# Kernel optimization log

Hardware: AMD Instinct MI355X
Metric: run time of the kernel (lower is better)

## Reference

```python
import jax, jax.numpy as jnp
import numpy as np

K_NN = 9  # neighbors including self (init kwarg K)
EPS = 1e-12  # F.normalize eps


def setup_inputs() -> dict:
    key = jax.random.key(0)
    ks = jax.random.split(key, 6)
    b, c, t = 8, 64, 4096
    c_out = 64
    x = jax.random.normal(ks[0], (b, c, t), dtype=jnp.float32)
    scale = 1.0 / np.sqrt(c)
    Wq = jax.random.normal(ks[1], (c, c), dtype=jnp.float32) * scale
    Wk = jax.random.normal(ks[2], (c, c), dtype=jnp.float32) * scale
    Wv = jax.random.normal(ks[3], (c, c), dtype=jnp.float32) * scale
    conv_w = jax.random.normal(ks[4], (c_out, c * K_NN), dtype=jnp.float32) * (1.0 / np.sqrt(c * K_NN))
    conv_b = jax.random.normal(ks[5], (c_out,), dtype=jnp.float32) * 0.01
    return {"x": x, "Wq": Wq, "Wk": Wk, "Wv": Wv, "conv_w": conv_w, "conv_b": conv_b}


def _l2norm_c(a):
    # normalize over channel dim (axis=1), matching F.normalize(p=2, dim=1)
    n = jnp.sqrt(jnp.sum(a * a, axis=1, keepdims=True))
    return a / jnp.maximum(n, EPS)


def reference(x, Wq, Wk, Wv, conv_w, conv_b):
    b, c, t = x.shape
    # QKV projections applied on channel dim: y[b,d,t] = sum_c W[d,c] * x[b,c,t]
    q = jnp.einsum('dc,bct->bdt', Wq, x)
    k = jnp.einsum('dc,bct->bdt', Wk, x)
    v = jnp.einsum('dc,bct->bdt', Wv, x)
    # cosine-similarity matrix [b, t, t]: sim[i, j] = k_i . q_j, clamped at 0
    sim = jnp.einsum('bci,bcj->bij', _l2norm_c(k), _l2norm_c(q))
    sim = jnp.maximum(sim, 0.0)
    # top-K neighbors (largest, since magnitude_type='similarity')
    _, idx = jax.lax.top_k(sim, K_NN)  # [b, t, K]
    # gather v at neighbor indices: prime[b,c,i,kk] = v[b,c, idx[b,i,kk]]
    gathered = jnp.take_along_axis(v[:, :, :, None], idx[:, None, :, :], axis=2)  # [b,c,t,K]
    # reshape to [b, c*K, t] (channel-major over K, matching the torch permute)
    prime = gathered.transpose(0, 1, 3, 2).reshape(b, c * K_NN, t)
    # 1x1 conv: out[b,o,t] = sum_k conv_w[o,k] * prime[b,k,t] + bias
    out = jnp.einsum('ok,bkt->bot', conv_w, prime) + conv_b[None, :, None]
    return out
```

## Files before the change

kernel.cpp:

```cpp
#include <hip/hip_runtime.h>
#include <hip/hip_bf16.h>
#include <cstdint>

#define BB  8
#define CH  64
#define TT  4096
#define KNN 9
#define NEG_INF (-3.402823466e38f)
#define SLOTS 96
#define SSTR  97
#define KTH   12

typedef short  s16x8 __attribute__((ext_vector_type(8)));
typedef float  f32x4 __attribute__((ext_vector_type(4)));

constexpr size_t OFF_UB  = 0;
constexpr size_t OFF_QTF = (size_t)BB*KNN*TT*CH/2;
constexpr size_t OFF_KTF = OFF_QTF + (size_t)BB*TT*CH;
constexpr size_t OFF_QTB = OFF_KTF + (size_t)BB*TT*CH;
constexpr size_t OFF_KTB = OFF_QTB + (size_t)BB*TT*CH/2;
constexpr size_t OFF_IDX = OFF_KTB + (size_t)BB*TT*CH/2;
constexpr size_t OFF_CWP = OFF_IDX + (size_t)BB*TT*KNN;

__device__ __forceinline__ unsigned short f2bf(float f) {
    unsigned u = __float_as_uint(f);
    return (unsigned short)((u + 0x7FFFu + ((u >> 16) & 1u)) >> 16);
}

__device__ __forceinline__ void insert2(float w, float (&s)[2]) {
    s[0] = __builtin_amdgcn_fmed3f(s[0], s[1], w);
    s[1] = fmaxf(s[1], w);
}

__device__ __forceinline__ float popTheta2(float (&s)[2], int lane) {
    float theta = NEG_INF;
    #pragma unroll 1
    for (int p = 0; p < KTH; ++p) {
        float h = s[1];
        float m = h;
        m = fmaxf(m, __shfl_xor(m, 1));
        m = fmaxf(m, __shfl_xor(m, 2));
        m = fmaxf(m, __shfl_xor(m, 4));
        m = fmaxf(m, __shfl_xor(m, 8));
        unsigned long long bal = __ballot(h == m);
        unsigned qb = (unsigned)((bal >> (lane & 48)) & 0xFFFFull);
        int owner = __ffs(qb) - 1;
        if ((lane & 15) == owner) {
            s[1] = s[0]; s[0] = NEG_INF;
        }
        theta = m;
    }
    return theta;
}

__device__ __forceinline__ void insert9x(float w, int wi, float (&s)[9], int (&si)[9]) {
    bool c[9];
    #pragma unroll
    for (int k = 0; k < 9; ++k) c[k] = (w > s[k]) || (w == s[k] && wi < si[k]);
    #pragma unroll
    for (int k = 0; k < 8; ++k) si[k] = c[k + 1] ? si[k + 1] : (c[k] ? wi : si[k]);
    si[8] = c[8] ? wi : si[8];
    #pragma unroll
    for (int k = 0; k < 8; ++k) s[k] = c[k + 1] ? s[k + 1] : (c[k] ? w : s[k]);
    s[8] = c[8] ? w : s[8];
}

__global__ void repack_cw_kernel(const float* __restrict__ cw, unsigned short* __restrict__ cwb) {
    int e = blockIdx.x * blockDim.x + threadIdx.x;
    if (e >= KNN * 4 * 2 * 64) return;
    int lane = e & 63;
    int ks   = (e >> 6) & 1;
    int ot   = (e >> 7) & 3;
    int kk   = e >> 9;
    int o    = ot * 16 + (lane & 15);
    int cc0  = ks * 32 + (lane >> 4) * 8;
    unsigned short* dst = cwb + (size_t)e * 8;
    #pragma unroll
    for (int i = 0; i < 8; ++i)
        dst[i] = f2bf(cw[o * (CH * KNN) + (cc0 + i) * KNN + kk]);
}

__global__ __launch_bounds__(512) void qkvu_kernel(
        const float* __restrict__ x,
        const float* __restrict__ Wq, const float* __restrict__ Wk, const float* __restrict__ Wv,
        const unsigned short* __restrict__ cwb,
        float* __restrict__ qtf, float* __restrict__ ktf,
        unsigned short* __restrict__ qtb, unsigned short* __restrict__ ktb,
        unsigned short* __restrict__ ub) {
    __shared__ __align__(16) float xs[CH * 64];
    __shared__ __align__(16) unsigned short vsb[64 * 64];
    __shared__ float pq[8 * 64], pk[8 * 64];

    const int b   = blockIdx.x >> 6;
    const int tb  = blockIdx.x & 63;
    const int tid = threadIdx.x;

    const float* xb = x + ((size_t)b * CH) * TT + tb * 64;
    #pragma unroll
    for (int m = 0; m < 8; ++m) {
        int l = tid + 512 * m;
        xs[l] = xb[(size_t)(l >> 6) * TT + (l & 63)];
    }
    __syncthreads();

    const int t = tid & 63;
    const int g = __builtin_amdgcn_readfirstlane(tid >> 6);
    const int d0 = g * 8;

    float qa[8], ka[8], va[8];
    #pragma unroll
    for (int dd = 0; dd < 8; ++dd) { qa[dd] = 0.f; ka[dd] = 0.f; va[dd] = 0.f; }

    #pragma unroll 4
    for (int c = 0; c < CH; ++c) {
        float xv = xs[c * 64 + t];
        #pragma unroll
        for (int dd = 0; dd < 8; ++dd) {
            qa[dd] = fmaf(Wq[(d0 + dd) * CH + c], xv, qa[dd]);
            ka[dd] = fmaf(Wk[(d0 + dd) * CH + c], xv, ka[dd]);
            va[dd] = fmaf(Wv[(d0 + dd) * CH + c], xv, va[dd]);
        }
    }

    float sq = 0.f, sk = 0.f;
    #pragma unroll
    for (int dd = 0; dd < 8; ++dd) { sq = fmaf(qa[dd], qa[dd], sq); sk = fmaf(ka[dd], ka[dd], sk); }
    pq[g * 64 + t] = sq;
    pk[g * 64 + t] = sk;
    __syncthreads();

    float nq2 = 0.f, nk2 = 0.f;
    #pragma unroll
    for (int p = 0; p < 8; ++p) { nq2 += pq[p * 64 + t]; nk2 += pk[p * 64 + t]; }
    const float isq = 1.0f / fmaxf(sqrtf(nq2), 1e-12f);
    const float isk = 1.0f / fmaxf(sqrtf(nk2), 1e-12f);

    const size_t tg = (size_t)tb * 64 + t;
    float qn[8], kn[8];
    #pragma unroll
    for (int dd = 0; dd < 8; ++dd) {
        qn[dd] = qa[dd] * isq;
        kn[dd] = ka[dd] * isk;
    }
    {
        unsigned* vh = (unsigned*)&vsb[t * 64 + d0];
        #pragma unroll
        for (int p = 0; p < 4; ++p)
            vh[p] = (unsigned)f2bf(va[2*p]) | ((unsigned)f2bf(va[2*p+1]) << 16);
    }
    float* qf = qtf + ((size_t)b * TT + tg) * CH + d0;
    float* kf = ktf + ((size_t)b * TT + tg) * CH + d0;
    #pragma unroll
    for (int p = 0; p < 2; ++p) {
        *(float4*)&qf[p * 4] = make_float4(qn[p*4], qn[p*4+1], qn[p*4+2], qn[p*4+3]);
        *(float4*)&kf[p * 4] = make_float4(kn[p*4], kn[p*4+1], kn[p*4+2], kn[p*4+3]);
    }
    {
        unsigned* kh = (unsigned*)(ktb + ((size_t)b * TT + tg) * CH + d0);
        #pragma unroll
        for (int p = 0; p < 4; ++p)
            kh[p] = (unsigned)f2bf(kn[2*p]) | ((unsigned)f2bf(kn[2*p+1]) << 16);
    }
    {
        const int j0   = (int)(tg >> 4);
        const int l15q = (int)tg & 15;
        const int ks   = g >> 2;
        const int qd   = g & 3;
        unsigned w0 = (unsigned)f2bf(qn[0]) | ((unsigned)f2bf(qn[1]) << 16);
        unsigned w1 = (unsigned)f2bf(qn[2]) | ((unsigned)f2bf(qn[3]) << 16);
        unsigned w2 = (unsigned)f2bf(qn[4]) | ((unsigned)f2bf(qn[5]) << 16);
        unsigned w3 = (unsigned)f2bf(qn[6]) | ((unsigned)f2bf(qn[7]) << 16);
        unsigned short* dst = qtb +
            ((((size_t)b * 256 + j0) * 2 + ks) * 64 + (qd * 16 + l15q)) * 8;
        *(uint4*)dst = make_uint4(w0, w1, w2, w3);
    }
    __syncthreads();

    const int l15 = t & 15;
    const int quad = t >> 4;
    const int rt4 = g & 3;
    const int oth = g >> 2;
    s16x8 av[2];
    #pragma unroll
    for (int ks = 0; ks < 2; ++ks)
        av[ks] = *(const s16x8*)&vsb[(rt4 * 16 + l15) * 64 + ks * 32 + quad * 8];

    #pragma unroll 1
    for (int kk = 0; kk < KNN; ++kk) {
        f32x4 ua[2];
        ua[0] = (f32x4){0.f, 0.f, 0.f, 0.f};
        ua[1] = (f32x4){0.f, 0.f, 0.f, 0.f};
        #pragma unroll
        for (int ks = 0; ks < 2; ++ks)
            #pragma unroll
            for (int oi = 0; oi < 2; ++oi) {
                const int ot = oth * 2 + oi;
                s16x8 bw = *(const s16x8*)(cwb + ((((size_t)kk * 4 + ot) * 2 + ks) * 64 + t) * 8);
                ua[oi] = __builtin_amdgcn_mfma_f32_16x16x32_bf16(av[ks], bw, ua[oi], 0, 0, 0);
            }
        const size_t rowb = (size_t)(b * KNN + kk) * TT + tb * 64 + rt4 * 16 + quad * 4;
        #pragma unroll
        for (int oi = 0; oi < 2; ++oi)
            #pragma unroll
            for (int r = 0; r < 4; ++r)
                ub[(rowb + r) * CH + (oth * 2 + oi) * 16 + l15] = f2bf(ua[oi][r]);
    }
}

__global__ __launch_bounds__(256, 2) void sim_topk_kernel(
        const unsigned short* __restrict__ qtb, const unsigned short* __restrict__ ktb,
        const float* __restrict__ qtf, const float* __restrict__ ktf,
        const unsigned short* __restrict__ ub, const float* __restrict__ conv_b,
        float* __restrict__ out) {
    __shared__ int   cnt[64];
    __shared__ int   bkt[64 * SSTR];
    __shared__ float wbf[64 * SSTR];
    __shared__ int   sidx[64 * KNN];

    const int b    = blockIdx.x & 7;
    const int ib   = blockIdx.x >> 3;
    const int tid  = threadIdx.x;
    const int lane = tid & 63;
    const int w    = tid >> 6;
    const int w2r  = w >> 1;
    const int w2c  = w & 1;
    const int quad = lane >> 4;
    const int l15  = lane & 15;

    if (tid < 64) cnt[tid] = 0;
    __syncthreads();

    const unsigned short* kb = ktb + ((size_t)b * TT + ib * 64 + w2r * 32) * CH;
    s16x8 ka[2][2];
    #pragma unroll
    for (int rt = 0; rt < 2; ++rt)
        #pragma unroll
        for (int ks = 0; ks < 2; ++ks)
            ka[rt][ks] = *(const s16x8*)(kb + (size_t)(rt * 16 + l15) * CH + ks * 32 + quad * 8);

    const unsigned short* qfb = qtb + (((size_t)b * 256 + (size_t)w2c * 128) * 2) * 512
                                + (size_t)lane * 8;

    float s[2][4][2];
    #pragma unroll
    for (int rt = 0; rt < 2; ++rt)
        #pragma unroll
        for (int rg = 0; rg < 4; ++rg) { s[rt][rg][0] = NEG_INF; s[rt][rg][1] = NEG_INF; }

    for (int jt = 0; jt < 16; ++jt) {
        const unsigned short* qrow = qfb + (size_t)(jt * 8) * 1024;
        s16x8 qf[8][2];
        #pragma unroll
        for (int jj = 0; jj < 8; ++jj)
            #pragma unroll
            for (int ks = 0; ks < 2; ++ks)
                qf[jj][ks] = *(const s16x8*)(qrow + (size_t)(jj * 2 + ks) * 512);

        f32x4 acc[2][8];
        #pragma unroll
        for (int rt = 0; rt < 2; ++rt)
            #pragma unroll
            for (int jj = 0; jj < 8; ++jj) acc[rt][jj] = (f32x4){0.f, 0.f, 0.f, 0.f};
        #pragma unroll
        for (int ks = 0; ks < 2; ++ks)
            #pragma unroll
            for (int rt = 0; rt < 2; ++rt)
                #pragma unroll
                for (int jj = 0; jj < 8; ++jj)
                    acc[rt][jj] = __builtin_amdgcn_mfma_f32_16x16x32_bf16(ka[rt][ks], qf[jj][ks], acc[rt][jj], 0, 0, 0);

        #pragma unroll
        for (int rt = 0; rt < 2; ++rt)
            #pragma unroll
            for (int jj = 0; jj < 8; ++jj) {
                insert2(acc[rt][jj][0], s[rt][0]);
                insert2(acc[rt][jj][1], s[rt][1]);
                insert2(acc[rt][jj][2], s[rt][2]);
                insert2(acc[rt][jj][3], s[rt][3]);
            }
    }

    float th[2][4];
    #pragma unroll
    for (int rt = 0; rt < 2; ++rt) {
        th[rt][0] = popTheta2(s[rt][0], lane);
        th[rt][1] = popTheta2(s[rt][1], lane);
        th[rt][2] = popTheta2(s[rt][2], lane);
        th[rt][3] = popTheta2(s[rt][3], lane);
    }

    for (int jt = 0; jt < 16; ++jt) {
        const unsigned short* qrow = qfb + (size_t)(jt * 8) * 1024;
        s16x8 qf[8][2];
        #pragma unroll
        for (int jj = 0; jj < 8; ++jj)
            #pragma unroll
            for (int ks = 0; ks < 2; ++ks)
                qf[jj][ks] = *(const s16x8*)(qrow + (size_t)(jj * 2 + ks) * 512);

        f32x4 acc[2][8];
        #pragma unroll
        for (int rt = 0; rt < 2; ++rt)
            #pragma unroll
            for (int jj = 0; jj < 8; ++jj) acc[rt][jj] = (f32x4){0.f, 0.f, 0.f, 0.f};
        #pragma unroll
        for (int ks = 0; ks < 2; ++ks)
            #pragma unroll
            for (int rt = 0; rt < 2; ++rt)
                #pragma unroll
                for (int jj = 0; jj < 8; ++jj)
                    acc[rt][jj] = __builtin_amdgcn_mfma_f32_16x16x32_bf16(ka[rt][ks], qf[jj][ks], acc[rt][jj], 0, 0, 0);

        #pragma unroll
        for (int rt = 0; rt < 2; ++rt)
            #pragma unroll
            for (int jj = 0; jj < 8; ++jj) {
                const int j = w2c * 2048 + jt * 128 + jj * 16 + l15;
                #pragma unroll
                for (int rg = 0; rg < 4; ++rg) {
                    if (acc[rt][jj][rg] >= th[rt][rg]) {
                        int rowl = w2r * 32 + rt * 16 + quad * 4 + rg;
                        int sl = atomicAdd(&cnt[rowl], 1);
                        if (sl < SLOTS) bkt[rowl * SSTR + sl] = j;
                    }
                }
            }
    }
    __syncthreads();

    {
        int r = tid >> 2, sub = tid & 3;
        int n = min(cnt[r], SLOTS);
        const float* krow = ktf + ((size_t)b * TT + ib * 64 + r) * CH;
        for (int m = sub; m < n; m += 4) {
            int j = bkt[r * SSTR + m];
            const float* qrow = qtf + ((size_t)b * TT + j) * CH;
            float wv = 0.f;
            #pragma unroll
            for (int c4 = 0; c4 < 16; ++c4) {
                float4 kv = *(const float4*)&krow[c4 * 4];
                float4 qv = *(const float4*)&qrow[c4 * 4];
                wv = fmaf(kv.x, qv.x, wv); wv = fmaf(kv.y, qv.y, wv);
                wv = fmaf(kv.z, qv.z, wv); wv = fmaf(kv.w, qv.w, wv);
            }
            wbf[r * SSTR + m] = wv;
        }
    }
    __syncthreads();

    if (tid < 64) {
        int n = min(cnt[tid], SLOTS);
        float s9[9]; int si9[9];
        #pragma unroll
        for (int k = 0; k < 9; ++k) { s9[k] = NEG_INF; si9[k] = 0x7fffffff; }
        #pragma unroll 1
        for (int m = 0; m < n; ++m) insert9x(wbf[tid * SSTR + m], bkt[tid * SSTR + m], s9, si9);
        #pragma unroll
        for (int m = 0; m < 9; ++m) sidx[tid * KNN + m] = si9[8 - m];
    }
    __syncthreads();

    {
        const int tl = tid & 63;
        const int og = tid >> 6;
        const int o0 = og * 16;

        float acc[16];
        #pragma unroll
        for (int q = 0; q < 16; ++q) acc[q] = conv_b[o0 + q];

        #pragma unroll
        for (int kk = 0; kk < KNN; ++kk) {
            int j = sidx[tl * KNN + kk];
            const unsigned short* up = ub + (((size_t)(b * KNN + kk)) * TT + j) * CH + o0;
            #pragma unroll
            for (int q8 = 0; q8 < 2; ++q8) {
                uint4 raw = *(const uint4*)&up[q8 * 8];
                unsigned rw[4] = {raw.x, raw.y, raw.z, raw.w};
                #pragma unroll
                for (int p = 0; p < 4; ++p) {
                    acc[q8 * 8 + 2 * p]     += __uint_as_float(rw[p] << 16);
                    acc[q8 * 8 + 2 * p + 1] += __uint_as_float(rw[p] & 0xFFFF0000u);
                }
            }
        }
        const int t = ib * 64 + tl;
        #pragma unroll
        for (int q = 0; q < 16; ++q)
            out[((size_t)b * CH + o0 + q) * TT + t] = acc[q];
    }
}

extern "C" void kernel_launch(void* const* d_in, const int* in_sizes, int n_in,
                              void* d_out, int out_size, void* d_ws, size_t ws_size,
                              hipStream_t stream) {
    const float* x   = (const float*)d_in[0];
    const float* Wq  = (const float*)d_in[1];
    const float* Wk  = (const float*)d_in[2];
    const float* Wv  = (const float*)d_in[3];
    const float* cw  = (const float*)d_in[4];
    const float* cbp = (const float*)d_in[5];

    float* ws = (float*)d_ws;
    unsigned short* ub  = (unsigned short*)(ws + OFF_UB);
    float* qtf          = ws + OFF_QTF;
    float* ktf          = ws + OFF_KTF;
    unsigned short* qtb = (unsigned short*)(ws + OFF_QTB);
    unsigned short* ktb = (unsigned short*)(ws + OFF_KTB);
    unsigned short* cwb = (unsigned short*)(ws + OFF_CWP);
    float* out          = (float*)d_out;

    repack_cw_kernel<<<(KNN * 4 * 2 * 64 + 255) / 256, 256, 0, stream>>>(cw, cwb);
    qkvu_kernel<<<BB * 64, 512, 0, stream>>>(x, Wq, Wk, Wv, cwb, qtf, ktf, qtb, ktb, ub);
    sim_topk_kernel<<<BB * 64, 256, 0, stream>>>(qtb, ktb, qtf, ktf, ub, cbp, out);
}
```

Measured before the change: 235.2 us.

## Halve QKV kernel token tile to 32 to double block count

The QKV/projection kernel now processes 32 tokens per block instead of 64, launching 1024 blocks instead of 512. Each thread computes 4 output channels instead of 8, with the partial norm reduction widened to 16 groups and the MFMA stage remapped so each wave handles one 16x16 output tile. The aim is better occupancy and latency hiding on a GPU with many CUs, at the cost of more redundant weight loads per token and narrower stores.

```diff
diff --git a/kernel.cpp b/kernel.cpp
--- a/kernel.cpp
+++ b/kernel.cpp
@@ -87,35 +87,35 @@
         float* __restrict__ qtf, float* __restrict__ ktf,
         unsigned short* __restrict__ qtb, unsigned short* __restrict__ ktb,
         unsigned short* __restrict__ ub) {
-    __shared__ __align__(16) float xs[CH * 64];
-    __shared__ __align__(16) unsigned short vsb[64 * 64];
-    __shared__ float pq[8 * 64], pk[8 * 64];
-
-    const int b   = blockIdx.x >> 6;
-    const int tb  = blockIdx.x & 63;
+    __shared__ __align__(16) float xs[CH * 32];
+    __shared__ __align__(16) unsigned short vsb[32 * 64];
+    __shared__ float pq[16 * 32], pk[16 * 32];
+
+    const int b   = blockIdx.x >> 7;
+    const int tb  = blockIdx.x & 127;
     const int tid = threadIdx.x;
 
-    const float* xb = x + ((size_t)b * CH) * TT + tb * 64;
-    #pragma unroll
-    for (int m = 0; m < 8; ++m) {
+    const float* xb = x + ((size_t)b * CH) * TT + tb * 32;
+    #pragma unroll
+    for (int m = 0; m < 4; ++m) {
         int l = tid + 512 * m;
-        xs[l] = xb[(size_t)(l >> 6) * TT + (l & 63)];
-    }
-    __syncthreads();
-
-    const int t = tid & 63;
-    const int g = __builtin_amdgcn_readfirstlane(tid >> 6);
-    const int d0 = g * 8;
-
-    float qa[8], ka[8], va[8];
-    #pragma unroll
-    for (int dd = 0; dd < 8; ++dd) { qa[dd] = 0.f; ka[dd] = 0.f; va[dd] = 0.f; }
+        xs[l] = xb[(size_t)(l >> 5) * TT + (l & 31)];
+    }
+    __syncthreads();
+
+    const int t  = tid & 31;
+    const int dg = __builtin_amdgcn_readfirstlane(tid >> 6) * 2 + ((tid >> 5) & 1);
+    const int d0 = dg * 4;
+
+    float qa[4], ka[4], va[4];
+    #pragma unroll
+    for (int dd = 0; dd < 4; ++dd) { qa[dd] = 0.f; ka[dd] = 0.f; va[dd] = 0.f; }
 
     #pragma unroll 4
     for (int c = 0; c < CH; ++c) {
-        float xv = xs[c * 64 + t];
-        #pragma unroll
-        for (int dd = 0; dd < 8; ++dd) {
+        float xv = xs[c * 32 + t];
+        #pragma unroll
+        for (int dd = 0; dd < 4; ++dd) {
             qa[dd] = fmaf(Wq[(d0 + dd) * CH + c], xv, qa[dd]);
             ka[dd] = fmaf(Wk[(d0 + dd) * CH + c], xv, ka[dd]);
             va[dd] = fmaf(Wv[(d0 + dd) * CH + c], xv, va[dd]);
@@ -124,86 +124,73 @@
 
     float sq = 0.f, sk = 0.f;
     #pragma unroll
-    for (int dd = 0; dd < 8; ++dd) { sq = fmaf(qa[dd], qa[dd], sq); sk = fmaf(ka[dd], ka[dd], sk); }
-    pq[g * 64 + t] = sq;
-    pk[g * 64 + t] = sk;
+    for (int dd = 0; dd < 4; ++dd) { sq = fmaf(qa[dd], qa[dd], sq); sk = fmaf(ka[dd], ka[dd], sk); }
+    pq[dg * 32 + t] = sq;
+    pk[dg * 32 + t] = sk;
     __syncthreads();
 
     float nq2 = 0.f, nk2 = 0.f;
     #pragma unroll
-    for (int p = 0; p < 8; ++p) { nq2 += pq[p * 64 + t]; nk2 += pk[p * 64 + t]; }
+    for (int p = 0; p < 16; ++p) { nq2 += pq[p * 32 + t]; nk2 += pk[p * 32 + t]; }
     const float isq = 1.0f / fmaxf(sqrtf(nq2), 1e-12f);
     const float isk = 1.0f / fmaxf(sqrtf(nk2), 1e-12f);
 
-    const size_t tg = (size_t)tb * 64 + t;
-    float qn[8], kn[8];
-    #pragma unroll
-    for (int dd = 0; dd < 8; ++dd) {
+    const size_t tg = (size_t)tb * 32 + t;
+    float qn[4], kn[4];
+    #pragma unroll
+    for (int dd = 0; dd < 4; ++dd) {
         qn[dd] = qa[dd] * isq;
         kn[dd] = ka[dd] * isk;
     }
     {
         unsigned* vh = (unsigned*)&vsb[t * 64 + d0];
-        #pragma unroll
-        for (int p = 0; p < 4; ++p)
-            vh[p] = (unsigned)f2bf(va[2*p]) | ((unsigned)f2bf(va[2*p+1]) << 16);
-    }
-    float* qf = qtf + ((size_t)b * TT + tg) * CH + d0;
-    float* kf = ktf + ((size_t)b * TT + tg) * CH + d0;
-    #pragma unroll
-    for (int p = 0; p < 2; ++p) {
-        *(float4*)&qf[p * 4] = make_float4(qn[p*4], qn[p*4+1], qn[p*4+2], qn[p*4+3]);
-        *(float4*)&kf[p * 4] = make_float4(kn[p*4], kn[p*4+1], kn[p*4+2], kn[p*4+3]);
-    }
+        vh[0] = (unsigned)f2bf(va[0]) | ((unsigned)f2bf(va[1]) << 16);
+        vh[1] = (unsigned)f2bf(va[2]) | ((unsigned)f2bf(va[3]) << 16);
+    }
+    *(float4*)(qtf + ((size_t)b * TT + tg) * CH + d0) = make_float4(qn[0], qn[1], qn[2], qn[3]);
+    *(float4*)(ktf + ((size_t)b * TT + tg) * CH + d0) = make_float4(kn[0], kn[1], kn[2], kn[3]);
     {
         unsigned* kh = (unsigned*)(ktb + ((size_t)b * TT + tg) * CH + d0);
-        #pragma unroll
-        for (int p = 0; p < 4; ++p)
-            kh[p] = (unsigned)f2bf(kn[2*p]) | ((unsigned)f2bf(kn[2*p+1]) << 16);
+        kh[0] = (unsigned)f2bf(kn[0]) | ((unsigned)f2bf(kn[1]) << 16);
+        kh[1] = (unsigned)f2bf(kn[2]) | ((unsigned)f2bf(kn[3]) << 16);
     }
     {
         const int j0   = (int)(tg >> 4);
         const int l15q = (int)tg & 15;
-        const int ks   = g >> 2;
-        const int qd   = g & 3;
+        const int g8   = dg >> 1;
+        const int ks   = g8 >> 2;
+        const int qd   = g8 & 3;
         unsigned w0 = (unsigned)f2bf(qn[0]) | ((unsigned)f2bf(qn[1]) << 16);
         unsigned w1 = (unsigned)f2bf(qn[2]) | ((unsigned)f2bf(qn[3]) << 16);
-        unsigned w2 = (unsigned)f2bf(qn[4]) | ((unsigned)f2bf(qn[5]) << 16);
-        unsigned w3 = (unsigned)f2bf(qn[6]) | ((unsigned)f2bf(qn[7]) << 16);
         unsigned short* dst = qtb +
-            ((((size_t)b * 256 + j0) * 2 + ks) * 64 + (qd * 16 + l15q)) * 8;
-        *(uint4*)dst = make_uint4(w0, w1, w2, w3);
-    }
-    __syncthreads();
-
-    const int l15 = t & 15;
-    const int quad = t >> 4;
-    const int rt4 = g & 3;
-    const int oth = g >> 2;
+            ((((size_t)b * 256 + j0) * 2 + ks) * 64 + (qd * 16 + l15q)) * 8 + (dg & 1) * 4;
+        *(uint2*)dst = make_uint2(w0, w1);
+    }
+    __syncthreads();
+
+    const int w    = __builtin_amdgcn_readfirstlane(tid >> 6);
+    const int lane = tid & 63;
+    const int l15  = lane & 15;
+    const int quad = lane >> 4;
+    const int rt   = w & 1;
+    const int ot   = w >> 1;
     s16x8 av[2];
     #pragma unroll
     for (int ks = 0; ks < 2; ++ks)
-        av[ks] = *(const s16x8*)&vsb[(rt4 * 16 + l15) * 64 + ks * 32 + quad * 8];
+        av[ks] = *(const s16x8*)&vsb[(rt * 16 + l15) * 64 + ks * 32 + quad * 8];
 
     #pragma unroll 1
     for (int kk = 0; kk < KNN; ++kk) {
-        f32x4 ua[2];
-        ua[0] = (f32x4){0.f, 0.f, 0.f, 0.f};
-        ua[1] = (f32x4){0.f, 0.f, 0.f, 0.f};
-        #pragma unroll
-        for (int ks = 0; ks < 2; ++ks)
-            #pragma unroll
-            for (int oi = 0; oi < 2; ++oi) {
-                const int ot = oth * 2 + oi;
-                s16x8 bw = *(const s16x8*)(cwb + ((((size_t)kk * 4 + ot) * 2 + ks) * 64 + t) * 8);
-                ua[oi] = __builtin_amdgcn_mfma_f32_16x16x32_bf16(av[ks], bw, ua[oi], 0, 0, 0);
-            }
-        const size_t rowb = (size_t)(b * KNN + kk) * TT + tb * 64 + rt4 * 16 + quad * 4;
-        #pragma unroll
-        for (int oi = 0; oi < 2; ++oi)
-            #pragma unroll
-            for (int r = 0; r < 4; ++r)
-                ub[(rowb + r) * CH + (oth * 2 + oi) * 16 + l15] = f2bf(ua[oi][r]);
+        f32x4 ua = (f32x4){0.f, 0.f, 0.f, 0.f};
+        #pragma unroll
+        for (int ks = 0; ks < 2; ++ks) {
+            s16x8 bw = *(const s16x8*)(cwb + ((((size_t)kk * 4 + ot) * 2 + ks) * 64 + lane) * 8);
+            ua = __builtin_amdgcn_mfma_f32_16x16x32_bf16(av[ks], bw, ua, 0, 0, 0);
+        }
+        const size_t rowb = (size_t)(b * KNN + kk) * TT + tb * 32 + rt * 16 + quad * 4;
+        #pragma unroll
+        for (int r = 0; r < 4; ++r)
+            ub[(rowb + r) * CH + ot * 16 + l15] = f2bf(ua[r]);
     }
 }
 
@@ -411,6 +398,6 @@
     float* out          = (float*)d_out;
 
     repack_cw_kernel<<<(KNN * 4 * 2 * 64 + 255) / 256, 256, 0, stream>>>(cw, cwb);
-    qkvu_kernel<<<BB * 64, 512, 0, stream>>>(x, Wq, Wk, Wv, cwb, qtf, ktf, qtb, ktb, ub);
+    qkvu_kernel<<<BB * 128, 512, 0, stream>>>(x, Wq, Wk, Wv, cwb, qtf, ktf, qtb, ktb, ub);
     sim_topk_kernel<<<BB * 64, 256, 0, stream>>>(qtb, ktb, qtf, ktf, ub, cbp, out);
 }
```

Result: slower. 261.0 us (+11.0%).
